# Performance work log

Hardware: AMD Instinct MI355X
Metric: run time of the kernel (lower is better)

## Reference

```python
import jax, jax.numpy as jnp
import numpy as np

NEG_SLOPE = 0.01  # torch LeakyReLU default
BN_EPS = 1e-5
K = 3              # kernel_size
GROUPS = 4         # inter_channels // group_channels = 64 // 16
GC = 16            # group_channels


def conv1x1(x, w, b):
    # x: [b,c,h,w], w: [o,c], b: [o]
    return jnp.einsum('bchw,oc->bohw', x, w) + b[None, :, None, None]


def conv3x3(x, w, b):
    # x: [b,c,h,w], w: [o,i,3,3]
    y = jax.lax.conv_general_dilated(x, w, (1, 1), 'SAME',
                                     dimension_numbers=('NCHW', 'OIHW', 'NCHW'))
    return y + b[None, :, None, None]


def pixel_shuffle(x, r):
    b, c, h, w = x.shape
    x = x.reshape(b, c // (r * r), r, r, h, w)
    x = x.transpose(0, 1, 4, 2, 5, 3)  # b, c/r2, h, r, w, r
    return x.reshape(b, c // (r * r), h * r, w * r)


def setup_inputs() -> dict:
    key = jax.random.key(0)
    ks = jax.random.split(key, 16)
    f32 = jnp.float32
    inp = {
        'high_level': jax.random.normal(ks[0], (4, 256, 128, 128), f32),
        'low_level': jax.random.normal(ks[1], (4, 64, 256, 256), f32),
        'emb': jax.random.normal(ks[2], (4, 256, 256, 256), f32),
        # reduce: 1x1 conv 128 -> 64
        'reduce_w': jax.random.normal(ks[3], (64, 128), f32) * (1.0 / np.sqrt(128)),
        'reduce_b': jnp.zeros((64,), f32),
        # conv1: 1x1 conv 64 -> 16
        'conv1_w': jax.random.normal(ks[4], (16, 64), f32) * (1.0 / np.sqrt(64)),
        'conv1_b': jnp.zeros((16,), f32),
        # embconv: 1x1 conv 256 -> 16
        'embconv_w': jax.random.normal(ks[5], (16, 256), f32) * (1.0 / np.sqrt(256)),
        'embconv_b': jnp.zeros((16,), f32),
        # conv2: 3x3 conv 16 -> 36 (= K*K*groups)
        'conv2_w': jax.random.normal(ks[6], (36, 16, 3, 3), f32) * (1.0 / np.sqrt(16 * 9)),
        'conv2_b': jnp.zeros((36,), f32),
        # out: 1x1 conv 64 -> 32 + BatchNorm(eval) + LeakyReLU
        'out_w': jax.random.normal(ks[7], (32, 64), f32) * (1.0 / np.sqrt(64)),
        'out_b': jnp.zeros((32,), f32),
        'bn_gamma': jnp.ones((32,), f32),
        'bn_beta': jnp.zeros((32,), f32),
        'bn_mean': jnp.zeros((32,), f32),
        'bn_var': jnp.ones((32,), f32),
    }
    return inp


def reference(high_level, low_level, emb,
              reduce_w, reduce_b, conv1_w, conv1_b,
              embconv_w, embconv_b, conv2_w, conv2_b,
              out_w, out_b, bn_gamma, bn_beta, bn_mean, bn_var):
    cat = jnp.concatenate([pixel_shuffle(high_level, 2), low_level], axis=1)
    cat = conv1x1(cat, reduce_w, reduce_b)  # [b, 64, h, w]

    pre = conv1x1(cat, conv1_w, conv1_b) + conv1x1(emb, embconv_w, embconv_b)
    weight = conv3x3(jax.nn.leaky_relu(pre, NEG_SLOPE), conv2_w, conv2_b)  # [b, 36, h, w]

    b, _, h, w = weight.shape
    weight = weight.reshape(b, GROUPS, K * K, h, w)

    cat_g = cat.reshape(b, GROUPS, GC, h, w)
    pad = K // 2
    padded = jnp.pad(cat_g, ((0, 0), (0, 0), (0, 0), (pad, pad), (pad, pad)))
    # patches[..., k, :, :] = shifted window, k = x + y*K (y outer, x inner)
    patches = jnp.stack([padded[..., y:y + h, x:x + w]
                         for y in range(K) for x in range(K)], axis=3)  # [b,g,gc,K*K,h,w]
    out = jnp.sum(weight[:, :, None] * patches, axis=3)  # [b,g,gc,h,w]
    out = out.reshape(b, GROUPS * GC, h, w)

    out = conv1x1(out, out_w, out_b)
    out = (out - bn_mean[None, :, None, None]) * (
        bn_gamma[None, :, None, None] / jnp.sqrt(bn_var[None, :, None, None] + BN_EPS)
    ) + bn_beta[None, :, None, None]
    return jax.nn.leaky_relu(out, NEG_SLOPE)
```

## Files before the change

kernel.cpp:

```cpp
#include <hip/hip_runtime.h>
#include <math.h>

#define LEAK 0.01f


#define WS_PRE_OFF 16777216
#define WS_W_OFF   20971520

__global__ __launch_bounds__(256) void k0_transpose(
    const float* __restrict__ reduce_w, const float* __restrict__ conv1_w,
    const float* __restrict__ embconv_w, const float* __restrict__ conv2_w,
    const float* __restrict__ out_w, float* __restrict__ wbuf) {
  int idx = blockIdx.x * 256 + threadIdx.x;
  if (idx < 8192) {
    int c = idx >> 6, o = idx & 63;
    wbuf[idx] = reduce_w[o * 128 + c];
  } else if (idx < 9216) {
    int i2 = idx - 8192; int c = i2 >> 4, j = i2 & 15;
    wbuf[idx] = conv1_w[j * 64 + c];
  } else if (idx < 13312) {
    int i2 = idx - 9216; int c = i2 >> 4, j = i2 & 15;
    wbuf[idx] = embconv_w[j * 256 + c];
  } else if (idx < 18496) {
    int i2 = idx - 13312;
    int o = i2 % 36; int r = i2 / 36; int i = r & 15; int kk = r >> 4;
    wbuf[idx] = conv2_w[(o * 16 + i) * 9 + kk];
  } else if (idx < 20544) {
    int i2 = idx - 18496; int c = i2 >> 5, o = i2 & 31;
    wbuf[idx] = out_w[o * 64 + c];
  }
}

__global__ __launch_bounds__(256) void ka_fused(
    const float* __restrict__ high, const float* __restrict__ low,
    const float* __restrict__ emb,
    const float* __restrict__ reduce_b, const float* __restrict__ conv1_b,
    const float* __restrict__ embconv_b,
    const float* __restrict__ wbuf,
    float* __restrict__ cat_out, float* __restrict__ pre_out) {
  const float* rwt = wbuf;
  const float* c1t = wbuf + 8192;
  const float* ect = wbuf + 9216;

  int pix = blockIdx.x * 256 + threadIdx.x;
  int b   = pix >> 16;
  int rem = pix & 65535;
  int y   = rem >> 8, x = rem & 255;

  float acc[64];
#pragma unroll
  for (int o = 0; o < 64; ++o) acc[o] = reduce_b[o];

  int lane_off = ((x & 1) << 14) + (x >> 1);
  int hb = (b * 256 + ((y & 1) << 1)) * 16384 + ((y >> 1) << 7);
#pragma unroll 4
  for (int c = 0; c < 64; ++c) {
    float xv = high[hb + c * 65536 + lane_off];
    const float* wr = rwt + c * 64;
#pragma unroll
    for (int o4 = 0; o4 < 16; ++o4) {
      float4 w = *(const float4*)(wr + o4 * 4);
      acc[o4 * 4 + 0] = fmaf(w.x, xv, acc[o4 * 4 + 0]);
      acc[o4 * 4 + 1] = fmaf(w.y, xv, acc[o4 * 4 + 1]);
      acc[o4 * 4 + 2] = fmaf(w.z, xv, acc[o4 * 4 + 2]);
      acc[o4 * 4 + 3] = fmaf(w.w, xv, acc[o4 * 4 + 3]);
    }
  }
  int lb = b * 64 * 65536 + rem;
#pragma unroll 4
  for (int c = 0; c < 64; ++c) {
    float xv = low[lb + c * 65536];
    const float* wr = rwt + (64 + c) * 64;
#pragma unroll
    for (int o4 = 0; o4 < 16; ++o4) {
      float4 w = *(const float4*)(wr + o4 * 4);
      acc[o4 * 4 + 0] = fmaf(w.x, xv, acc[o4 * 4 + 0]);
      acc[o4 * 4 + 1] = fmaf(w.y, xv, acc[o4 * 4 + 1]);
      acc[o4 * 4 + 2] = fmaf(w.z, xv, acc[o4 * 4 + 2]);
      acc[o4 * 4 + 3] = fmaf(w.w, xv, acc[o4 * 4 + 3]);
    }
  }

  {
    float* cp = cat_out + (size_t)pix * 64;
#pragma unroll
    for (int o4 = 0; o4 < 16; ++o4) {
      float4 v;
      v.x = acc[o4 * 4 + 0]; v.y = acc[o4 * 4 + 1];
      v.z = acc[o4 * 4 + 2]; v.w = acc[o4 * 4 + 3];
      *(float4*)(cp + o4 * 4) = v;
    }
  }

  float pre[16];
#pragma unroll
  for (int j = 0; j < 16; ++j) pre[j] = conv1_b[j] + embconv_b[j];

#pragma unroll
  for (int c = 0; c < 64; ++c) {
    float xv = acc[c];
    const float* wr = c1t + c * 16;
#pragma unroll
    for (int j4 = 0; j4 < 4; ++j4) {
      float4 w = *(const float4*)(wr + j4 * 4);
      pre[j4 * 4 + 0] = fmaf(w.x, xv, pre[j4 * 4 + 0]);
      pre[j4 * 4 + 1] = fmaf(w.y, xv, pre[j4 * 4 + 1]);
      pre[j4 * 4 + 2] = fmaf(w.z, xv, pre[j4 * 4 + 2]);
      pre[j4 * 4 + 3] = fmaf(w.w, xv, pre[j4 * 4 + 3]);
    }
  }

  int eb = b * 256 * 65536 + rem;
#pragma unroll 4
  for (int c = 0; c < 256; ++c) {
    float xv = emb[eb + c * 65536];
    const float* wr = ect + c * 16;
#pragma unroll
    for (int j4 = 0; j4 < 4; ++j4) {
      float4 w = *(const float4*)(wr + j4 * 4);
      pre[j4 * 4 + 0] = fmaf(w.x, xv, pre[j4 * 4 + 0]);
      pre[j4 * 4 + 1] = fmaf(w.y, xv, pre[j4 * 4 + 1]);
      pre[j4 * 4 + 2] = fmaf(w.z, xv, pre[j4 * 4 + 2]);
      pre[j4 * 4 + 3] = fmaf(w.w, xv, pre[j4 * 4 + 3]);
    }
  }

  {
    float* pp = pre_out + (size_t)pix * 16;
#pragma unroll
    for (int j4 = 0; j4 < 4; ++j4) {
      float4 v;
      float a0 = pre[j4 * 4 + 0], a1 = pre[j4 * 4 + 1];
      float a2 = pre[j4 * 4 + 2], a3 = pre[j4 * 4 + 3];
      v.x = a0 > 0.f ? a0 : a0 * LEAK;
      v.y = a1 > 0.f ? a1 : a1 * LEAK;
      v.z = a2 > 0.f ? a2 : a2 * LEAK;
      v.w = a3 > 0.f ? a3 : a3 * LEAK;
      *(float4*)(pp + j4 * 4) = v;
    }
  }
}

__global__ __launch_bounds__(256) void kb_fused(
    const float* __restrict__ cat_in, const float* __restrict__ pre_in,
    const float* __restrict__ wbuf,
    const float* __restrict__ conv2_b, const float* __restrict__ out_b,
    const float* __restrict__ bn_gamma, const float* __restrict__ bn_beta,
    const float* __restrict__ bn_mean, const float* __restrict__ bn_var,
    float* __restrict__ out) {
  const float* w2t = wbuf + 13312;
  const float* owt = wbuf + 18496;

  __shared__ float lds_pre[16][324];

  int tid = threadIdx.x;
  int bx = blockIdx.x & 15, by = (blockIdx.x >> 4) & 15, b = blockIdx.x >> 8;
  int x0 = bx << 4, y0 = by << 4;
  int tx = tid & 15, ty = tid >> 4;

  for (int s = tid; s < 324; s += 256) {
    int sy = s / 18, sx = s - sy * 18;
    int gy = y0 + sy - 1, gx = x0 + sx - 1;
    float4 p0 = {0.f, 0.f, 0.f, 0.f}, p1 = p0, p2 = p0, p3 = p0;
    if ((unsigned)gy < 256u && (unsigned)gx < 256u) {
      const float* pp = pre_in + (size_t)((b * 256 + gy) * 256 + gx) * 16;
      p0 = *(const float4*)(pp + 0);
      p1 = *(const float4*)(pp + 4);
      p2 = *(const float4*)(pp + 8);
      p3 = *(const float4*)(pp + 12);
    }
    lds_pre[0][s] = p0.x;  lds_pre[1][s] = p0.y;
    lds_pre[2][s] = p0.z;  lds_pre[3][s] = p0.w;
    lds_pre[4][s] = p1.x;  lds_pre[5][s] = p1.y;
    lds_pre[6][s] = p1.z;  lds_pre[7][s] = p1.w;
    lds_pre[8][s] = p2.x;  lds_pre[9][s] = p2.y;
    lds_pre[10][s] = p2.z; lds_pre[11][s] = p2.w;
    lds_pre[12][s] = p3.x; lds_pre[13][s] = p3.y;
    lds_pre[14][s] = p3.z; lds_pre[15][s] = p3.w;
  }
  __syncthreads();

  int px = x0 + tx, py = y0 + ty;

  float wgt[36];
#pragma unroll
  for (int o = 0; o < 36; ++o) wgt[o] = conv2_b[o];

  for (int k = 0; k < 9; ++k) {
    int ky = k / 3, kx = k - ky * 3;
    int slot = (ty + ky) * 18 + (tx + kx);
    float pv[16];
#pragma unroll
    for (int i = 0; i < 16; ++i) pv[i] = lds_pre[i][slot];
    const float* wp = w2t + k * 576;
#pragma unroll
    for (int i = 0; i < 16; ++i) {
      float xv = pv[i];
#pragma unroll
      for (int o4 = 0; o4 < 9; ++o4) {
        float4 w = *(const float4*)(wp + i * 36 + o4 * 4);
        wgt[o4 * 4 + 0] = fmaf(w.x, xv, wgt[o4 * 4 + 0]);
        wgt[o4 * 4 + 1] = fmaf(w.y, xv, wgt[o4 * 4 + 1]);
        wgt[o4 * 4 + 2] = fmaf(w.z, xv, wgt[o4 * 4 + 2]);
        wgt[o4 * 4 + 3] = fmaf(w.w, xv, wgt[o4 * 4 + 3]);
      }
    }
  }

  float agg[64];
#pragma unroll
  for (int c = 0; c < 64; ++c) agg[c] = 0.f;

#pragma unroll
  for (int k = 0; k < 9; ++k) {
    int ky = k / 3, kx = k - ky * 3;
    int gy = py + ky - 1, gx = px + kx - 1;
    bool valid = ((unsigned)gy < 256u) && ((unsigned)gx < 256u);
    int cgy = gy < 0 ? 0 : (gy > 255 ? 255 : gy);
    int cgx = gx < 0 ? 0 : (gx > 255 ? 255 : gx);
    const float* cp = cat_in + (size_t)((b * 256 + cgy) * 256 + cgx) * 64;
    float wk0 = valid ? wgt[0 * 9 + k] : 0.f;
    float wk1 = valid ? wgt[1 * 9 + k] : 0.f;
    float wk2 = valid ? wgt[2 * 9 + k] : 0.f;
    float wk3 = valid ? wgt[3 * 9 + k] : 0.f;
#pragma unroll
    for (int c4 = 0; c4 < 16; ++c4) {
      float4 cv = *(const float4*)(cp + c4 * 4);
      float wk = (c4 < 4) ? wk0 : (c4 < 8) ? wk1 : (c4 < 12) ? wk2 : wk3;
      agg[c4 * 4 + 0] = fmaf(wk, cv.x, agg[c4 * 4 + 0]);
      agg[c4 * 4 + 1] = fmaf(wk, cv.y, agg[c4 * 4 + 1]);
      agg[c4 * 4 + 2] = fmaf(wk, cv.z, agg[c4 * 4 + 2]);
      agg[c4 * 4 + 3] = fmaf(wk, cv.w, agg[c4 * 4 + 3]);
    }
  }

  float o32[32];
#pragma unroll
  for (int o = 0; o < 32; ++o) o32[o] = out_b[o];
#pragma unroll
  for (int c = 0; c < 64; ++c) {
    float xv = agg[c];
    const float* wr = owt + c * 32;
#pragma unroll
    for (int o4 = 0; o4 < 8; ++o4) {
      float4 w = *(const float4*)(wr + o4 * 4);
      o32[o4 * 4 + 0] = fmaf(w.x, xv, o32[o4 * 4 + 0]);
      o32[o4 * 4 + 1] = fmaf(w.y, xv, o32[o4 * 4 + 1]);
      o32[o4 * 4 + 2] = fmaf(w.z, xv, o32[o4 * 4 + 2]);
      o32[o4 * 4 + 3] = fmaf(w.w, xv, o32[o4 * 4 + 3]);
    }
  }

  int outbase = (b * 32 * 256 + py) * 256 + px;
#pragma unroll
  for (int o = 0; o < 32; ++o) {
    float sc = bn_gamma[o] / sqrtf(bn_var[o] + 1e-5f);
    float v = (o32[o] - bn_mean[o]) * sc + bn_beta[o];
    v = v > 0.f ? v : v * LEAK;
    out[outbase + o * 65536] = v;
  }
}

extern "C" void kernel_launch(void* const* d_in, const int* in_sizes, int n_in,
                              void* d_out, int out_size, void* d_ws, size_t ws_size,
                              hipStream_t stream) {
  const float* high      = (const float*)d_in[0];
  const float* low       = (const float*)d_in[1];
  const float* emb       = (const float*)d_in[2];
  const float* reduce_w  = (const float*)d_in[3];
  const float* reduce_b  = (const float*)d_in[4];
  const float* conv1_w   = (const float*)d_in[5];
  const float* conv1_b   = (const float*)d_in[6];
  const float* embconv_w = (const float*)d_in[7];
  const float* embconv_b = (const float*)d_in[8];
  const float* conv2_w   = (const float*)d_in[9];
  const float* conv2_b   = (const float*)d_in[10];
  const float* out_w     = (const float*)d_in[11];
  const float* out_b     = (const float*)d_in[12];
  const float* bn_gamma  = (const float*)d_in[13];
  const float* bn_beta   = (const float*)d_in[14];
  const float* bn_mean   = (const float*)d_in[15];
  const float* bn_var    = (const float*)d_in[16];

  float* ws   = (float*)d_ws;
  float* cat  = ws;
  float* pre  = ws + WS_PRE_OFF;
  float* wbuf = ws + WS_W_OFF;

  k0_transpose<<<81, 256, 0, stream>>>(reduce_w, conv1_w, embconv_w, conv2_w,
                                       out_w, wbuf);
  ka_fused<<<1024, 256, 0, stream>>>(high, low, emb, reduce_b, conv1_b,
                                     embconv_b, wbuf, cat, pre);
  kb_fused<<<1024, 256, 0, stream>>>(cat, pre, wbuf, conv2_b, out_b, bn_gamma,
                                     bn_beta, bn_mean, bn_var, (float*)d_out);
}
```

Baseline: 701.4 us.

## Group-major cat layout with LDS halo tiles; fold BatchNorm into out weights

Stores the intermediate cat tensor as per-group planes of 16 channels and, in the second kernel, stages each group's 18x18 halo tile into shared memory with float4 loads. Each neighbour is then read from LDS rather than reloaded from global memory nine times, and the agg accumulator shrinks to 16 registers. The pre tile moves to a padded pixel-major LDS layout so it can be read with float4. BatchNorm scale and shift are folded into the output conv weights and bias in the setup kernel, and the unroll of the first kernel's channel loops goes from 4 to 8. In exchange there are extra block-wide barriers per group, and the wider unroll may raise register pressure.

```diff
diff --git a/kernel.cpp b/kernel.cpp
--- a/kernel.cpp
+++ b/kernel.cpp
@@ -2,7 +2,6 @@
 #include <math.h>
 
 #define LEAK 0.01f
-
 
 #define WS_PRE_OFF 16777216
 #define WS_W_OFF   20971520
@@ -10,7 +9,10 @@
 __global__ __launch_bounds__(256) void k0_transpose(
     const float* __restrict__ reduce_w, const float* __restrict__ conv1_w,
     const float* __restrict__ embconv_w, const float* __restrict__ conv2_w,
-    const float* __restrict__ out_w, float* __restrict__ wbuf) {
+    const float* __restrict__ out_w, const float* __restrict__ out_b,
+    const float* __restrict__ bn_gamma, const float* __restrict__ bn_beta,
+    const float* __restrict__ bn_mean, const float* __restrict__ bn_var,
+    float* __restrict__ wbuf) {
   int idx = blockIdx.x * 256 + threadIdx.x;
   if (idx < 8192) {
     int c = idx >> 6, o = idx & 63;
@@ -27,7 +29,12 @@
     wbuf[idx] = conv2_w[(o * 16 + i) * 9 + kk];
   } else if (idx < 20544) {
     int i2 = idx - 18496; int c = i2 >> 5, o = i2 & 31;
-    wbuf[idx] = out_w[o * 64 + c];
+    float sc = bn_gamma[o] * rsqrtf(bn_var[o] + 1e-5f);
+    wbuf[idx] = out_w[o * 64 + c] * sc;
+  } else if (idx < 20576) {
+    int o = idx - 20544;
+    float sc = bn_gamma[o] * rsqrtf(bn_var[o] + 1e-5f);
+    wbuf[idx] = (out_b[o] - bn_mean[o]) * sc + bn_beta[o];
   }
 }
 
@@ -53,7 +60,7 @@
 
   int lane_off = ((x & 1) << 14) + (x >> 1);
   int hb = (b * 256 + ((y & 1) << 1)) * 16384 + ((y >> 1) << 7);
-#pragma unroll 4
+#pragma unroll 8
   for (int c = 0; c < 64; ++c) {
     float xv = high[hb + c * 65536 + lane_off];
     const float* wr = rwt + c * 64;
@@ -67,7 +74,7 @@
     }
   }
   int lb = b * 64 * 65536 + rem;
-#pragma unroll 4
+#pragma unroll 8
   for (int c = 0; c < 64; ++c) {
     float xv = low[lb + c * 65536];
     const float* wr = rwt + (64 + c) * 64;
@@ -81,13 +88,14 @@
     }
   }
 
-  {
-    float* cp = cat_out + (size_t)pix * 64;
-#pragma unroll
-    for (int o4 = 0; o4 < 16; ++o4) {
+#pragma unroll
+  for (int g = 0; g < 4; ++g) {
+    float* cp = cat_out + (((size_t)(b * 4 + g) << 16) + rem) * 16;
+#pragma unroll
+    for (int o4 = 0; o4 < 4; ++o4) {
       float4 v;
-      v.x = acc[o4 * 4 + 0]; v.y = acc[o4 * 4 + 1];
-      v.z = acc[o4 * 4 + 2]; v.w = acc[o4 * 4 + 3];
+      v.x = acc[g * 16 + o4 * 4 + 0]; v.y = acc[g * 16 + o4 * 4 + 1];
+      v.z = acc[g * 16 + o4 * 4 + 2]; v.w = acc[g * 16 + o4 * 4 + 3];
       *(float4*)(cp + o4 * 4) = v;
     }
   }
@@ -111,7 +119,7 @@
   }
 
   int eb = b * 256 * 65536 + rem;
-#pragma unroll 4
+#pragma unroll 8
   for (int c = 0; c < 256; ++c) {
     float xv = emb[eb + c * 65536];
     const float* wr = ect + c * 16;
@@ -144,43 +152,29 @@
 __global__ __launch_bounds__(256) void kb_fused(
     const float* __restrict__ cat_in, const float* __restrict__ pre_in,
     const float* __restrict__ wbuf,
-    const float* __restrict__ conv2_b, const float* __restrict__ out_b,
-    const float* __restrict__ bn_gamma, const float* __restrict__ bn_beta,
-    const float* __restrict__ bn_mean, const float* __restrict__ bn_var,
+    const float* __restrict__ conv2_b,
     float* __restrict__ out) {
-  const float* w2t = wbuf + 13312;
-  const float* owt = wbuf + 18496;
-
-  __shared__ float lds_pre[16][324];
+  const float* w2t   = wbuf + 13312;
+  const float* owt   = wbuf + 18496;
+  const float* obias = wbuf + 20544;
+
+  __shared__ __align__(16) float lds[324 * 20];
 
   int tid = threadIdx.x;
   int bx = blockIdx.x & 15, by = (blockIdx.x >> 4) & 15, b = blockIdx.x >> 8;
   int x0 = bx << 4, y0 = by << 4;
   int tx = tid & 15, ty = tid >> 4;
 
-  for (int s = tid; s < 324; s += 256) {
-    int sy = s / 18, sx = s - sy * 18;
+  for (int t = tid; t < 1296; t += 256) {
+    int site = t >> 2, part = t & 3;
+    int sy = site / 18, sx = site - sy * 18;
     int gy = y0 + sy - 1, gx = x0 + sx - 1;
-    float4 p0 = {0.f, 0.f, 0.f, 0.f}, p1 = p0, p2 = p0, p3 = p0;
-    if ((unsigned)gy < 256u && (unsigned)gx < 256u) {
-      const float* pp = pre_in + (size_t)((b * 256 + gy) * 256 + gx) * 16;
-      p0 = *(const float4*)(pp + 0);
-      p1 = *(const float4*)(pp + 4);
-      p2 = *(const float4*)(pp + 8);
-      p3 = *(const float4*)(pp + 12);
-    }
-    lds_pre[0][s] = p0.x;  lds_pre[1][s] = p0.y;
-    lds_pre[2][s] = p0.z;  lds_pre[3][s] = p0.w;
-    lds_pre[4][s] = p1.x;  lds_pre[5][s] = p1.y;
-    lds_pre[6][s] = p1.z;  lds_pre[7][s] = p1.w;
-    lds_pre[8][s] = p2.x;  lds_pre[9][s] = p2.y;
-    lds_pre[10][s] = p2.z; lds_pre[11][s] = p2.w;
-    lds_pre[12][s] = p3.x; lds_pre[13][s] = p3.y;
-    lds_pre[14][s] = p3.z; lds_pre[15][s] = p3.w;
+    float4 v = {0.f, 0.f, 0.f, 0.f};
+    if ((unsigned)gy < 256u && (unsigned)gx < 256u)
+      v = *(const float4*)(pre_in + ((size_t)((b << 16) + gy * 256 + gx)) * 16 + part * 4);
+    *(float4*)(lds + site * 20 + part * 4) = v;
   }
   __syncthreads();
-
-  int px = x0 + tx, py = y0 + ty;
 
   float wgt[36];
 #pragma unroll
@@ -189,9 +183,13 @@
   for (int k = 0; k < 9; ++k) {
     int ky = k / 3, kx = k - ky * 3;
     int slot = (ty + ky) * 18 + (tx + kx);
-    float pv[16];
-#pragma unroll
-    for (int i = 0; i < 16; ++i) pv[i] = lds_pre[i][slot];
+    const float* lp = lds + slot * 20;
+    float4 q0 = *(const float4*)(lp + 0);
+    float4 q1 = *(const float4*)(lp + 4);
+    float4 q2 = *(const float4*)(lp + 8);
+    float4 q3 = *(const float4*)(lp + 12);
+    float pv[16] = {q0.x, q0.y, q0.z, q0.w, q1.x, q1.y, q1.z, q1.w,
+                    q2.x, q2.y, q2.z, q2.w, q3.x, q3.y, q3.z, q3.w};
     const float* wp = w2t + k * 576;
 #pragma unroll
     for (int i = 0; i < 16; ++i) {
@@ -207,55 +205,69 @@
     }
   }
 
-  float agg[64];
-#pragma unroll
-  for (int c = 0; c < 64; ++c) agg[c] = 0.f;
-
-#pragma unroll
-  for (int k = 0; k < 9; ++k) {
-    int ky = k / 3, kx = k - ky * 3;
-    int gy = py + ky - 1, gx = px + kx - 1;
-    bool valid = ((unsigned)gy < 256u) && ((unsigned)gx < 256u);
-    int cgy = gy < 0 ? 0 : (gy > 255 ? 255 : gy);
-    int cgx = gx < 0 ? 0 : (gx > 255 ? 255 : gx);
-    const float* cp = cat_in + (size_t)((b * 256 + cgy) * 256 + cgx) * 64;
-    float wk0 = valid ? wgt[0 * 9 + k] : 0.f;
-    float wk1 = valid ? wgt[1 * 9 + k] : 0.f;
-    float wk2 = valid ? wgt[2 * 9 + k] : 0.f;
-    float wk3 = valid ? wgt[3 * 9 + k] : 0.f;
-#pragma unroll
-    for (int c4 = 0; c4 < 16; ++c4) {
-      float4 cv = *(const float4*)(cp + c4 * 4);
-      float wk = (c4 < 4) ? wk0 : (c4 < 8) ? wk1 : (c4 < 12) ? wk2 : wk3;
-      agg[c4 * 4 + 0] = fmaf(wk, cv.x, agg[c4 * 4 + 0]);
-      agg[c4 * 4 + 1] = fmaf(wk, cv.y, agg[c4 * 4 + 1]);
-      agg[c4 * 4 + 2] = fmaf(wk, cv.z, agg[c4 * 4 + 2]);
-      agg[c4 * 4 + 3] = fmaf(wk, cv.w, agg[c4 * 4 + 3]);
-    }
-  }
-
   float o32[32];
 #pragma unroll
-  for (int o = 0; o < 32; ++o) o32[o] = out_b[o];
-#pragma unroll
-  for (int c = 0; c < 64; ++c) {
-    float xv = agg[c];
-    const float* wr = owt + c * 32;
-#pragma unroll
-    for (int o4 = 0; o4 < 8; ++o4) {
-      float4 w = *(const float4*)(wr + o4 * 4);
-      o32[o4 * 4 + 0] = fmaf(w.x, xv, o32[o4 * 4 + 0]);
-      o32[o4 * 4 + 1] = fmaf(w.y, xv, o32[o4 * 4 + 1]);
-      o32[o4 * 4 + 2] = fmaf(w.z, xv, o32[o4 * 4 + 2]);
-      o32[o4 * 4 + 3] = fmaf(w.w, xv, o32[o4 * 4 + 3]);
-    }
-  }
-
-  int outbase = (b * 32 * 256 + py) * 256 + px;
+  for (int o = 0; o < 32; ++o) o32[o] = obias[o];
+
+#pragma unroll
+  for (int g = 0; g < 4; ++g) {
+    __syncthreads();
+    for (int t = tid; t < 1296; t += 256) {
+      int site = t >> 2, part = t & 3;
+      int sy = site / 18, sx = site - sy * 18;
+      int gy = y0 + sy - 1, gx = x0 + sx - 1;
+      float4 v = {0.f, 0.f, 0.f, 0.f};
+      if ((unsigned)gy < 256u && (unsigned)gx < 256u)
+        v = *(const float4*)(cat_in +
+              (((size_t)(b * 4 + g) << 16) + gy * 256 + gx) * 16 + part * 4);
+      *(float4*)(lds + site * 20 + part * 4) = v;
+    }
+    __syncthreads();
+
+    float agg[16];
+#pragma unroll
+    for (int c = 0; c < 16; ++c) agg[c] = 0.f;
+
+#pragma unroll
+    for (int k = 0; k < 9; ++k) {
+      const int ky = k / 3, kx = k - ky * 3;
+      int slot = (ty + ky) * 18 + (tx + kx);
+      const float* lp = lds + slot * 20;
+      float4 c0 = *(const float4*)(lp + 0);
+      float4 c1 = *(const float4*)(lp + 4);
+      float4 c2 = *(const float4*)(lp + 8);
+      float4 c3 = *(const float4*)(lp + 12);
+      float wk = wgt[g * 9 + k];
+      agg[0]  = fmaf(wk, c0.x, agg[0]);  agg[1]  = fmaf(wk, c0.y, agg[1]);
+      agg[2]  = fmaf(wk, c0.z, agg[2]);  agg[3]  = fmaf(wk, c0.w, agg[3]);
+      agg[4]  = fmaf(wk, c1.x, agg[4]);  agg[5]  = fmaf(wk, c1.y, agg[5]);
+      agg[6]  = fmaf(wk, c1.z, agg[6]);  agg[7]  = fmaf(wk, c1.w, agg[7]);
+      agg[8]  = fmaf(wk, c2.x, agg[8]);  agg[9]  = fmaf(wk, c2.y, agg[9]);
+      agg[10] = fmaf(wk, c2.z, agg[10]); agg[11] = fmaf(wk, c2.w, agg[11]);
+      agg[12] = fmaf(wk, c3.x, agg[12]); agg[13] = fmaf(wk, c3.y, agg[13]);
+      agg[14] = fmaf(wk, c3.z, agg[14]); agg[15] = fmaf(wk, c3.w, agg[15]);
+    }
+
+#pragma unroll
+    for (int c = 0; c < 16; ++c) {
+      float xv = agg[c];
+      const float* wr = owt + (g * 16 + c) * 32;
+#pragma unroll
+      for (int o4 = 0; o4 < 8; ++o4) {
+        float4 w = *(const float4*)(wr + o4 * 4);
+        o32[o4 * 4 + 0] = fmaf(w.x, xv, o32[o4 * 4 + 0]);
+        o32[o4 * 4 + 1] = fmaf(w.y, xv, o32[o4 * 4 + 1]);
+        o32[o4 * 4 + 2] = fmaf(w.z, xv, o32[o4 * 4 + 2]);
+        o32[o4 * 4 + 3] = fmaf(w.w, xv, o32[o4 * 4 + 3]);
+      }
+    }
+  }
+
+  int px = x0 + tx, py = y0 + ty;
+  int outbase = ((b << 5) * 256 + py) * 256 + px;
 #pragma unroll
   for (int o = 0; o < 32; ++o) {
-    float sc = bn_gamma[o] / sqrtf(bn_var[o] + 1e-5f);
-    float v = (o32[o] - bn_mean[o]) * sc + bn_beta[o];
+    float v = o32[o];
     v = v > 0.f ? v : v * LEAK;
     out[outbase + o * 65536] = v;
   }
@@ -288,9 +300,9 @@
   float* wbuf = ws + WS_W_OFF;
 
   k0_transpose<<<81, 256, 0, stream>>>(reduce_w, conv1_w, embconv_w, conv2_w,
-                                       out_w, wbuf);
+                                       out_w, out_b, bn_gamma, bn_beta,
+                                       bn_mean, bn_var, wbuf);
   ka_fused<<<1024, 256, 0, stream>>>(high, low, emb, reduce_b, conv1_b,
                                      embconv_b, wbuf, cat, pre);
-  kb_fused<<<1024, 256, 0, stream>>>(cat, pre, wbuf, conv2_b, out_b, bn_gamma,
-                                     bn_beta, bn_mean, bn_var, (float*)d_out);
+  kb_fused<<<1024, 256, 0, stream>>>(cat, pre, wbuf, conv2_b, (float*)d_out);
 }
```

After: 806.5 us. +15.0%, slower.
